# Kernel tuning notes

Measured on AMD Instinct MI355X. Metric: run time of the kernel, lower is better.

The kernel has to match this reference:

```python
import jax, jax.numpy as jnp
import numpy as np

NUM_Q = 10000
DK = 128   # dim_key (width of each memory slot and of embeddings)
DV = 64    # dim_value (number of memory slots)
B = 128
S = 200


def setup_inputs() -> dict:
    key = jax.random.key(0)
    ks = jax.random.split(key, 16)
    sc = 0.05
    return {
        "question_seq": jax.random.randint(ks[0], (B, S), 0, NUM_Q),
        "correct_seq": jax.random.randint(ks[1], (B, S), 0, 2),
        "k_emb": jax.random.normal(ks[2], (NUM_Q, DK), jnp.float32) * sc,
        "v_emb": jax.random.normal(ks[3], (2 * NUM_Q, DK), jnp.float32) * sc,
        "Mk": jax.random.normal(ks[4], (DV, DK), jnp.float32) * sc,
        "Mv0": jax.random.normal(ks[5], (DV, DK), jnp.float32) * sc,
        "fW": jax.random.normal(ks[6], (2 * DK, DK), jnp.float32) * sc,
        "fb": jnp.zeros((DK,), jnp.float32),
        "eW": jax.random.normal(ks[7], (DK, DK), jnp.float32) * sc,
        "eb": jnp.zeros((DK,), jnp.float32),
        "aW": jax.random.normal(ks[8], (DK, DK), jnp.float32) * sc,
        "ab": jnp.zeros((DK,), jnp.float32),
        "pW": jax.random.normal(ks[9], (DK, 1), jnp.float32) * sc,
        "pb": jnp.zeros((1,), jnp.float32),
    }


def reference(question_seq, correct_seq, k_emb, v_emb, Mk, Mv0, fW, fb, eW, eb, aW, ab, pW, pb):
    num_q = k_emb.shape[0]
    x = question_seq + num_q * correct_seq            # [B,S]
    k = k_emb[question_seq]                           # [B,S,DK]
    v = v_emb[x]                                      # [B,S,DK]

    w = jax.nn.softmax(jnp.einsum('bsk,vk->bsv', k, Mk), axis=-1)  # [B,S,DV]
    e = jax.nn.sigmoid(v @ eW + eb)                   # [B,S,DK]
    a = jnp.tanh(v @ aW + ab)                         # [B,S,DK]

    Mvt0 = jnp.broadcast_to(Mv0[None], (question_seq.shape[0],) + Mv0.shape)  # [B,DV,DK]

    def step(Mvt, inp):
        wt, et, at = inp                              # [B,DV],[B,DK],[B,DK]
        read = jnp.einsum('bv,bvk->bk', wt, Mvt)      # read BEFORE update (Mv[:, :-1])
        we = wt[:, :, None] * et[:, None, :]          # [B,DV,DK]
        wa = wt[:, :, None] * at[:, None, :]
        Mvt_new = Mvt * (1.0 - we) + wa
        return Mvt_new, read

    xs = (w.transpose(1, 0, 2), e.transpose(1, 0, 2), a.transpose(1, 0, 2))
    _, reads = jax.lax.scan(step, Mvt0, xs)           # reads: [S,B,DK]
    reads = reads.transpose(1, 0, 2)                  # [B,S,DK]

    f = jnp.tanh(jnp.concatenate([reads, k], axis=-1) @ fW + fb)  # [B,S,DK]
    # dropout is identity in eval mode
    predict_score = jax.nn.sigmoid(f @ pW + pb).squeeze(-1)       # [B,S]
    return predict_score
```

## Files before the change

### kernel.cpp

```cpp
#include <hip/hip_runtime.h>
#include <math.h>


typedef float f32x4 __attribute__((ext_vector_type(4)));
typedef short bf16x8 __attribute__((ext_vector_type(8)));

__device__ __forceinline__ float sigm(float x) { return 1.0f / (1.0f + __expf(-x)); }
__device__ __forceinline__ short f2bf(float x) {
    union { float f; unsigned u; } v; v.f = x;
    return (short)((v.u + 0x7FFFu + ((v.u >> 16) & 1u)) >> 16);
}

__global__ __launch_bounds__(128) void prep_kernel(
    const float* __restrict__ eW, const float* __restrict__ aW,
    const float* __restrict__ fW, const float* __restrict__ Mk,
    short* __restrict__ eWt, short* __restrict__ aWt,
    short* __restrict__ fWrt, short* __restrict__ fWkt,
    short* __restrict__ Mkb)
{
    const int t = threadIdx.x;
    if (blockIdx.x == 4) {
        for (int idx = t; idx < 1024; idx += 128) {
            const int row = idx >> 4, c8 = idx & 15;
            const float4 f0 = *(const float4*)(Mk + row * 128 + c8 * 8);
            const float4 f1 = *(const float4*)(Mk + row * 128 + c8 * 8 + 4);
            bf16x8 v;
            v[0] = f2bf(f0.x); v[1] = f2bf(f0.y); v[2] = f2bf(f0.z); v[3] = f2bf(f0.w);
            v[4] = f2bf(f1.x); v[5] = f2bf(f1.y); v[6] = f2bf(f1.z); v[7] = f2bf(f1.w);
            *(bf16x8*)(Mkb + row * 128 + c8 * 8) = v;
        }
        return;
    }
    const float* src; short* dst;
    switch (blockIdx.x) {
        case 0:  src = eW;             dst = eWt;  break;
        case 1:  src = aW;             dst = aWt;  break;
        case 2:  src = fW;             dst = fWrt; break;
        default: src = fW + 128 * 128; dst = fWkt; break;
    }
    const int n = t;
    for (int k0 = 0; k0 < 128; k0 += 8) {
        bf16x8 v;
        #pragma unroll
        for (int kk = 0; kk < 8; ++kk) v[kk] = f2bf(src[(k0 + kk) * 128 + n]);
        *(bf16x8*)(dst + n * 128 + k0) = v;
    }
}

__global__ __launch_bounds__(256) void veakf_kernel(
    const float* __restrict__ v_emb, const float* __restrict__ k_emb,
    const short* __restrict__ eWt, const short* __restrict__ aWt,
    const short* __restrict__ fWkt, const short* __restrict__ Mkb,
    const float* __restrict__ eb, const float* __restrict__ ab,
    const float* __restrict__ fb,
    int num_q, int nbe,
    float* __restrict__ e_all, float* __restrict__ a_all,
    float* __restrict__ kf_all, float* __restrict__ w_all)
{
    __shared__ __align__(16) short Ash[64 * 128];
    const int t = threadIdx.x;
    const bool ea = ((int)blockIdx.x < nbe);
    const int nrows = ea ? 2 * num_q : num_q;
    const int R0 = (ea ? blockIdx.x : blockIdx.x - nbe) * 64;
    const float* Asrc = ea ? v_emb : k_emb;

    #pragma unroll
    for (int i = 0; i < 4; ++i) {
        const int c = t + 256 * i;
        const int row = c >> 4, ch = c & 15;
        int gr = R0 + row; if (gr > nrows - 1) gr = nrows - 1;
        const float4 f0 = *(const float4*)(Asrc + (size_t)gr * 128 + ch * 8);
        const float4 f1 = *(const float4*)(Asrc + (size_t)gr * 128 + ch * 8 + 4);
        bf16x8 v;
        v[0] = f2bf(f0.x); v[1] = f2bf(f0.y); v[2] = f2bf(f0.z); v[3] = f2bf(f0.w);
        v[4] = f2bf(f1.x); v[5] = f2bf(f1.y); v[6] = f2bf(f1.z); v[7] = f2bf(f1.w);
        *(bf16x8*)&Ash[row * 128 + ((ch ^ (row & 7)) * 8)] = v;
    }
    __syncthreads();

    const int wv = t >> 6;
    const int lr = t & 15;
    const int lk = (t & 63) >> 4;
    const int arow = wv * 16 + lr;

    if (ea) {
        f32x4 acc0[8], acc1[8];
        #pragma unroll
        for (int ct = 0; ct < 8; ++ct) { acc0[ct] = (f32x4)0.f; acc1[ct] = (f32x4)0.f; }
        #pragma unroll
        for (int ks = 0; ks < 4; ++ks) {
            const int chunk = ks * 4 + lk;
            const bf16x8 af = *(const bf16x8*)&Ash[arow * 128 + ((chunk ^ (arow & 7)) * 8)];
            const int kb = ks * 32 + lk * 8;
            #pragma unroll
            for (int ct = 0; ct < 8; ++ct) {
                const int n = ct * 16 + lr;
                const bf16x8 b0 = *(const bf16x8*)(eWt + n * 128 + kb);
                const bf16x8 b1 = *(const bf16x8*)(aWt + n * 128 + kb);
                acc0[ct] = __builtin_amdgcn_mfma_f32_16x16x32_bf16(af, b0, acc0[ct], 0, 0, 0);
                acc1[ct] = __builtin_amdgcn_mfma_f32_16x16x32_bf16(af, b1, acc1[ct], 0, 0, 0);
            }
        }
        #pragma unroll
        for (int ct = 0; ct < 8; ++ct) {
            const int col = ct * 16 + lr;
            const float ebv = eb[col], abv = ab[col];
            #pragma unroll
            for (int r = 0; r < 4; ++r) {
                const int row = R0 + wv * 16 + lk * 4 + r;
                if (row < nrows) {
                    e_all[(size_t)row * 128 + col] = sigm(acc0[ct][r] + ebv);
                    a_all[(size_t)row * 128 + col] = tanhf(acc1[ct][r] + abv);
                }
            }
        }
    } else {
        f32x4 acc0[8], accw[4];
        #pragma unroll
        for (int ct = 0; ct < 8; ++ct) acc0[ct] = (f32x4)0.f;
        #pragma unroll
        for (int ct = 0; ct < 4; ++ct) accw[ct] = (f32x4)0.f;
        #pragma unroll
        for (int ks = 0; ks < 4; ++ks) {
            const int chunk = ks * 4 + lk;
            const bf16x8 af = *(const bf16x8*)&Ash[arow * 128 + ((chunk ^ (arow & 7)) * 8)];
            const int kb = ks * 32 + lk * 8;
            #pragma unroll
            for (int ct = 0; ct < 8; ++ct) {
                const int n = ct * 16 + lr;
                const bf16x8 b0 = *(const bf16x8*)(fWkt + n * 128 + kb);
                acc0[ct] = __builtin_amdgcn_mfma_f32_16x16x32_bf16(af, b0, acc0[ct], 0, 0, 0);
            }
            #pragma unroll
            for (int ct = 0; ct < 4; ++ct) {
                const int n = ct * 16 + lr;
                const bf16x8 bm = *(const bf16x8*)(Mkb + n * 128 + kb);
                accw[ct] = __builtin_amdgcn_mfma_f32_16x16x32_bf16(af, bm, accw[ct], 0, 0, 0);
            }
        }
        #pragma unroll
        for (int ct = 0; ct < 8; ++ct) {
            const int col = ct * 16 + lr;
            const float fbv = fb[col];
            #pragma unroll
            for (int r = 0; r < 4; ++r) {
                const int row = R0 + wv * 16 + lk * 4 + r;
                if (row < nrows)
                    kf_all[(size_t)row * 128 + col] = acc0[ct][r] + fbv;
            }
        }
        #pragma unroll
        for (int r = 0; r < 4; ++r) {
            const float x0 = accw[0][r], x1 = accw[1][r];
            const float x2 = accw[2][r], x3 = accw[3][r];
            float m = fmaxf(fmaxf(x0, x1), fmaxf(x2, x3));
            #pragma unroll
            for (int mk = 1; mk < 16; mk <<= 1) m = fmaxf(m, __shfl_xor(m, mk));
            const float e0 = __expf(x0 - m), e1 = __expf(x1 - m);
            const float e2 = __expf(x2 - m), e3 = __expf(x3 - m);
            float s = (e0 + e1) + (e2 + e3);
            #pragma unroll
            for (int mk = 1; mk < 16; mk <<= 1) s += __shfl_xor(s, mk);
            const float inv = 1.0f / s;
            const int row = R0 + wv * 16 + lk * 4 + r;
            if (row < nrows) {
                float* wr = w_all + (size_t)row * 64 + lr;
                wr[0]  = e0 * inv; wr[16] = e1 * inv;
                wr[32] = e2 * inv; wr[48] = e3 * inv;
            }
        }
    }
}

__global__ __launch_bounds__(256) void scan_kernel(
    const float* __restrict__ Mv0,
    const int* __restrict__ qseq, const int* __restrict__ cseq,
    const float* __restrict__ w_all, const float* __restrict__ e_all,
    const float* __restrict__ a_all, int num_q,
    unsigned short* __restrict__ reads_bf)
{
    const int t  = threadIdx.x;
    const int j  = t & 31;
    const int vg = t >> 5;
    const int cq = blockIdx.x & 3;
    const int b  = blockIdx.x >> 2;
    const int jg = cq * 32 + j;

    float Mv[8];
    #pragma unroll
    for (int i = 0; i < 8; ++i) Mv[i] = Mv0[(vg * 8 + i) * 128 + jg];

    __shared__ float wb[2][8][64];
    __shared__ float ebuf[2][8][32];
    __shared__ float abuf[2][8][32];
    __shared__ float part[2][8][8][32];
    __shared__ int sq[200], sx[200];

    if (t < 200) {
        const int q = qseq[b * 200 + t];
        const int c = cseq[b * 200 + t];
        sq[t] = q * 16;
        sx[t] = (q + num_q * c) * 32 + cq * 8;
    }
    __syncthreads();

    const float4* w4 = (const float4*)w_all;
    const float4* e4 = (const float4*)e_all;
    const float4* a4 = (const float4*)a_all;
    unsigned short* rp = reads_bf + (size_t)b * 200 * 128 + jg;

    float4 rg;
    if (t < 128)      { rg = w4[sq[t >> 4] + (t & 15)];               ((float4*)wb[0])[t] = rg; }
    else if (t < 192) { const int u = t - 128; rg = e4[sx[u >> 3] + (u & 7)]; ((float4*)ebuf[0])[u] = rg; }
    else              { const int u = t - 192; rg = a4[sx[u >> 3] + (u & 7)]; ((float4*)abuf[0])[u] = rg; }
    __syncthreads();

    int cb = 0, pbuf = 0;
    for (int c = 0; c < 25; ++c) {
        if (c < 24) {
            const int s0 = (c + 1) * 8;
            if (t < 128)      rg = w4[sq[s0 + (t >> 4)] + (t & 15)];
            else if (t < 192) { const int u = t - 128; rg = e4[sx[s0 + (u >> 3)] + (u & 7)]; }
            else              { const int u = t - 192; rg = a4[sx[s0 + (u >> 3)] + (u & 7)]; }
        }
        #pragma unroll
        for (int st = 0; st < 8; ++st) {
            const float e_j = ebuf[cb][st][j];
            const float a_j = abuf[cb][st][j];
            const float* wrow = &wb[cb][st][vg * 8];
            float r0 = 0.f, r1 = 0.f, r2 = 0.f, r3 = 0.f;
            #pragma unroll
            for (int v4i = 0; v4i < 2; ++v4i) {
                const float4 w4v = *(const float4*)&wrow[v4i * 4];
                const int v = v4i * 4;
                r0 = fmaf(w4v.x, Mv[v + 0], r0);
                Mv[v + 0] = fmaf(w4v.x, fmaf(-Mv[v + 0], e_j, a_j), Mv[v + 0]);
                r1 = fmaf(w4v.y, Mv[v + 1], r1);
                Mv[v + 1] = fmaf(w4v.y, fmaf(-Mv[v + 1], e_j, a_j), Mv[v + 1]);
                r2 = fmaf(w4v.z, Mv[v + 2], r2);
                Mv[v + 2] = fmaf(w4v.z, fmaf(-Mv[v + 2], e_j, a_j), Mv[v + 2]);
                r3 = fmaf(w4v.w, Mv[v + 3], r3);
                Mv[v + 3] = fmaf(w4v.w, fmaf(-Mv[v + 3], e_j, a_j), Mv[v + 3]);
            }
            part[pbuf][st][vg][j] = (r0 + r1) + (r2 + r3);
        }
        if (c < 24) {
            if (t < 128)      ((float4*)wb[cb ^ 1])[t] = rg;
            else if (t < 192) ((float4*)ebuf[cb ^ 1])[t - 128] = rg;
            else              ((float4*)abuf[cb ^ 1])[t - 192] = rg;
        }
        __syncthreads();
        {
            const int st = t >> 5, jr = t & 31;
            const float* pp = &part[pbuf][st][0][jr];
            float r = 0.f;
            #pragma unroll
            for (int g = 0; g < 8; ++g) r += pp[g * 32];
            reads_bf[(size_t)b * 200 * 128 + (size_t)(c * 8 + st) * 128 + cq * 32 + jr]
                = (unsigned short)f2bf(r);
        }
        cb ^= 1; pbuf ^= 1;
    }
    (void)rp;
}

__global__ __launch_bounds__(256) void out_kernel(
    const int* __restrict__ qseq,
    const unsigned short* __restrict__ reads_bf,
    const short* __restrict__ fWrt, const float* __restrict__ kf_all,
    const float* __restrict__ pW, const float* __restrict__ pb,
    int ntok, float* __restrict__ out)
{
    __shared__ __align__(16) short Ash[64 * 128];
    __shared__ int qi[64];
    const int t = threadIdx.x;
    const int R0 = blockIdx.x * 64;
    if (t < 64) { int r = R0 + t; qi[t] = qseq[r < ntok ? r : ntok - 1]; }
    #pragma unroll
    for (int i = 0; i < 4; ++i) {
        const int c = t + 256 * i;
        const int row = c >> 4, ch = c & 15;
        int gr = R0 + row; if (gr > ntok - 1) gr = ntok - 1;
        const bf16x8 v = *(const bf16x8*)(reads_bf + (size_t)gr * 128 + ch * 8);
        *(bf16x8*)&Ash[row * 128 + ((ch ^ (row & 7)) * 8)] = v;
    }
    __syncthreads();

    const int wv = t >> 6;
    const int lr = t & 15;
    const int lk = (t & 63) >> 4;
    const int arow = wv * 16 + lr;

    f32x4 acc[8];
    #pragma unroll
    for (int ct = 0; ct < 8; ++ct) {
        const int col = ct * 16 + lr;
        #pragma unroll
        for (int r = 0; r < 4; ++r) {
            const int q = qi[wv * 16 + lk * 4 + r];
            acc[ct][r] = kf_all[(size_t)q * 128 + col];
        }
    }
    #pragma unroll
    for (int ks = 0; ks < 4; ++ks) {
        const int chunk = ks * 4 + lk;
        const bf16x8 af = *(const bf16x8*)&Ash[arow * 128 + ((chunk ^ (arow & 7)) * 8)];
        const int kb = ks * 32 + lk * 8;
        #pragma unroll
        for (int ct = 0; ct < 8; ++ct) {
            const int n = ct * 16 + lr;
            const bf16x8 bfr = *(const bf16x8*)(fWrt + n * 128 + kb);
            acc[ct] = __builtin_amdgcn_mfma_f32_16x16x32_bf16(af, bfr, acc[ct], 0, 0, 0);
        }
    }
    const float pb0 = pb[0];
    float s0 = 0.f, s1 = 0.f, s2 = 0.f, s3 = 0.f;
    #pragma unroll
    for (int ct = 0; ct < 8; ++ct) {
        const float pw = pW[ct * 16 + lr];
        s0 = fmaf(tanhf(acc[ct][0]), pw, s0);
        s1 = fmaf(tanhf(acc[ct][1]), pw, s1);
        s2 = fmaf(tanhf(acc[ct][2]), pw, s2);
        s3 = fmaf(tanhf(acc[ct][3]), pw, s3);
    }
    #pragma unroll
    for (int off = 1; off < 16; off <<= 1) {
        s0 += __shfl_xor(s0, off);
        s1 += __shfl_xor(s1, off);
        s2 += __shfl_xor(s2, off);
        s3 += __shfl_xor(s3, off);
    }
    if (lr == 0) {
        const int row = R0 + wv * 16 + lk * 4;
        if (row + 0 < ntok) out[row + 0] = sigm(s0 + pb0);
        if (row + 1 < ntok) out[row + 1] = sigm(s1 + pb0);
        if (row + 2 < ntok) out[row + 2] = sigm(s2 + pb0);
        if (row + 3 < ntok) out[row + 3] = sigm(s3 + pb0);
    }
}

extern "C" void kernel_launch(void* const* d_in, const int* in_sizes, int n_in,
                              void* d_out, int out_size, void* d_ws, size_t ws_size,
                              hipStream_t stream)
{
    const int*   qseq  = (const int*)d_in[0];
    const int*   cseq  = (const int*)d_in[1];
    const float* k_emb = (const float*)d_in[2];
    const float* v_emb = (const float*)d_in[3];
    const float* Mk    = (const float*)d_in[4];
    const float* Mv0   = (const float*)d_in[5];
    const float* fW    = (const float*)d_in[6];
    const float* fb    = (const float*)d_in[7];
    const float* eW    = (const float*)d_in[8];
    const float* eb    = (const float*)d_in[9];
    const float* aW    = (const float*)d_in[10];
    const float* ab    = (const float*)d_in[11];
    const float* pW    = (const float*)d_in[12];
    const float* pb    = (const float*)d_in[13];

    const int num_q = in_sizes[2] / 128;
    const int ntok  = in_sizes[0];
    const int Bb    = ntok / 200;
    const int NV    = 2 * num_q;

    float* ws = (float*)d_ws;
    float* w_all  = ws;
    float* e_all  = w_all  + (size_t)num_q * 64;
    float* a_all  = e_all  + (size_t)NV * 128;
    float* kf_all = a_all  + (size_t)NV * 128;
    short* eWt    = (short*)(kf_all + (size_t)num_q * 128);
    short* aWt    = eWt  + 128 * 128;
    short* fWrt   = aWt  + 128 * 128;
    short* fWkt   = fWrt + 128 * 128;
    short* Mkb    = fWkt + 128 * 128;
    unsigned short* reads_bf = (unsigned short*)(Mkb + 64 * 128);

    prep_kernel<<<5, 128, 0, stream>>>(eW, aW, fW, Mk, eWt, aWt, fWrt, fWkt, Mkb);
    const int nbe = (NV + 63) / 64, nbk = (num_q + 63) / 64;
    veakf_kernel<<<nbe + nbk, 256, 0, stream>>>(v_emb, k_emb, eWt, aWt, fWkt, Mkb,
                                                eb, ab, fb, num_q, nbe,
                                                e_all, a_all, kf_all, w_all);
    scan_kernel<<<Bb * 4, 256, 0, stream>>>(Mv0, qseq, cseq, w_all, e_all, a_all,
                                            num_q, reads_bf);
    out_kernel<<<(ntok + 63) / 64, 256, 0, stream>>>(qseq, reads_bf, fWrt, kf_all,
                                                     pW, pb, ntok, (float*)d_out);
}
```

Baseline: 77.56 us.

## Stage weight matrices in LDS and load activation fragments directly to registers

```diff
diff --git a/kernel.cpp b/kernel.cpp
--- a/kernel.cpp
+++ b/kernel.cpp
@@ -11,7 +11,7 @@
     return (short)((v.u + 0x7FFFu + ((v.u >> 16) & 1u)) >> 16);
 }
 
-__global__ __launch_bounds__(128) void prep_kernel(
+__global__ __launch_bounds__(256) void prep_kernel(
     const float* __restrict__ eW, const float* __restrict__ aW,
     const float* __restrict__ fW, const float* __restrict__ Mk,
     short* __restrict__ eWt, short* __restrict__ aWt,
@@ -20,7 +20,7 @@
 {
     const int t = threadIdx.x;
     if (blockIdx.x == 4) {
-        for (int idx = t; idx < 1024; idx += 128) {
+        for (int idx = t; idx < 1024; idx += 256) {
             const int row = idx >> 4, c8 = idx & 15;
             const float4 f0 = *(const float4*)(Mk + row * 128 + c8 * 8);
             const float4 f1 = *(const float4*)(Mk + row * 128 + c8 * 8 + 4);
@@ -38,8 +38,9 @@
         case 2:  src = fW;             dst = fWrt; break;
         default: src = fW + 128 * 128; dst = fWkt; break;
     }
-    const int n = t;
-    for (int k0 = 0; k0 < 128; k0 += 8) {
+    const int n  = t & 127;
+    const int kh = (t >> 7) * 64;
+    for (int k0 = kh; k0 < kh + 64; k0 += 8) {
         bf16x8 v;
         #pragma unroll
         for (int kk = 0; kk < 8; ++kk) v[kk] = f2bf(src[(k0 + kk) * 128 + n]);
@@ -57,87 +58,74 @@
     float* __restrict__ e_all, float* __restrict__ a_all,
     float* __restrict__ kf_all, float* __restrict__ w_all)
 {
-    __shared__ __align__(16) short Ash[64 * 128];
+    __shared__ __align__(16) short Bsh[128 * 128];
     const int t = threadIdx.x;
     const bool ea = ((int)blockIdx.x < nbe);
     const int nrows = ea ? 2 * num_q : num_q;
-    const int R0 = (ea ? blockIdx.x : blockIdx.x - nbe) * 64;
+    const int R0 = (ea ? (int)blockIdx.x : (int)blockIdx.x - nbe) * 64;
     const float* Asrc = ea ? v_emb : k_emb;
-
-    #pragma unroll
-    for (int i = 0; i < 4; ++i) {
-        const int c = t + 256 * i;
-        const int row = c >> 4, ch = c & 15;
-        int gr = R0 + row; if (gr > nrows - 1) gr = nrows - 1;
-        const float4 f0 = *(const float4*)(Asrc + (size_t)gr * 128 + ch * 8);
-        const float4 f1 = *(const float4*)(Asrc + (size_t)gr * 128 + ch * 8 + 4);
-        bf16x8 v;
-        v[0] = f2bf(f0.x); v[1] = f2bf(f0.y); v[2] = f2bf(f0.z); v[3] = f2bf(f0.w);
-        v[4] = f2bf(f1.x); v[5] = f2bf(f1.y); v[6] = f2bf(f1.z); v[7] = f2bf(f1.w);
-        *(bf16x8*)&Ash[row * 128 + ((ch ^ (row & 7)) * 8)] = v;
-    }
-    __syncthreads();
 
     const int wv = t >> 6;
     const int lr = t & 15;
     const int lk = (t & 63) >> 4;
     const int arow = wv * 16 + lr;
-
+    int gr = R0 + arow; if (gr > nrows - 1) gr = nrows - 1;
+
+    float4 a0[4], a1[4];
+    #pragma unroll
+    for (int ks = 0; ks < 4; ++ks) {
+        const int off = (ks * 4 + lk) * 8;
+        a0[ks] = *(const float4*)(Asrc + (size_t)gr * 128 + off);
+        a1[ks] = *(const float4*)(Asrc + (size_t)gr * 128 + off + 4);
+    }
+    {
+        const short* B1 = ea ? eWt : fWkt;
+        #pragma unroll
+        for (int i = 0; i < 8; ++i) {
+            const int c = t + 256 * i;
+            const int row = c >> 4, ch = c & 15;
+            *(bf16x8*)&Bsh[row * 128 + ((ch ^ (row & 7)) * 8)] =
+                *(const bf16x8*)(B1 + row * 128 + ch * 8);
+        }
+    }
+    bf16x8 af[4];
+    #pragma unroll
+    for (int ks = 0; ks < 4; ++ks) {
+        bf16x8 v;
+        v[0] = f2bf(a0[ks].x); v[1] = f2bf(a0[ks].y);
+        v[2] = f2bf(a0[ks].z); v[3] = f2bf(a0[ks].w);
+        v[4] = f2bf(a1[ks].x); v[5] = f2bf(a1[ks].y);
+        v[6] = f2bf(a1[ks].z); v[7] = f2bf(a1[ks].w);
+        af[ks] = v;
+    }
+    __syncthreads();
+
+    f32x4 acc[8];
+    #pragma unroll
+    for (int ct = 0; ct < 8; ++ct) acc[ct] = (f32x4)0.f;
+    #pragma unroll
+    for (int ks = 0; ks < 4; ++ks) {
+        const int chunk = ks * 4 + lk;
+        #pragma unroll
+        for (int ct = 0; ct < 8; ++ct) {
+            const int n = ct * 16 + lr;
+            const bf16x8 b = *(const bf16x8*)&Bsh[n * 128 + ((chunk ^ (n & 7)) * 8)];
+            acc[ct] = __builtin_amdgcn_mfma_f32_16x16x32_bf16(af[ks], b, acc[ct], 0, 0, 0);
+        }
+    }
     if (ea) {
-        f32x4 acc0[8], acc1[8];
-        #pragma unroll
-        for (int ct = 0; ct < 8; ++ct) { acc0[ct] = (f32x4)0.f; acc1[ct] = (f32x4)0.f; }
-        #pragma unroll
-        for (int ks = 0; ks < 4; ++ks) {
-            const int chunk = ks * 4 + lk;
-            const bf16x8 af = *(const bf16x8*)&Ash[arow * 128 + ((chunk ^ (arow & 7)) * 8)];
-            const int kb = ks * 32 + lk * 8;
-            #pragma unroll
-            for (int ct = 0; ct < 8; ++ct) {
-                const int n = ct * 16 + lr;
-                const bf16x8 b0 = *(const bf16x8*)(eWt + n * 128 + kb);
-                const bf16x8 b1 = *(const bf16x8*)(aWt + n * 128 + kb);
-                acc0[ct] = __builtin_amdgcn_mfma_f32_16x16x32_bf16(af, b0, acc0[ct], 0, 0, 0);
-                acc1[ct] = __builtin_amdgcn_mfma_f32_16x16x32_bf16(af, b1, acc1[ct], 0, 0, 0);
-            }
-        }
         #pragma unroll
         for (int ct = 0; ct < 8; ++ct) {
             const int col = ct * 16 + lr;
-            const float ebv = eb[col], abv = ab[col];
+            const float ebv = eb[col];
             #pragma unroll
             for (int r = 0; r < 4; ++r) {
                 const int row = R0 + wv * 16 + lk * 4 + r;
-                if (row < nrows) {
-                    e_all[(size_t)row * 128 + col] = sigm(acc0[ct][r] + ebv);
-                    a_all[(size_t)row * 128 + col] = tanhf(acc1[ct][r] + abv);
-                }
+                if (row < nrows)
+                    e_all[(size_t)row * 128 + col] = sigm(acc[ct][r] + ebv);
             }
         }
     } else {
-        f32x4 acc0[8], accw[4];
-        #pragma unroll
-        for (int ct = 0; ct < 8; ++ct) acc0[ct] = (f32x4)0.f;
-        #pragma unroll
-        for (int ct = 0; ct < 4; ++ct) accw[ct] = (f32x4)0.f;
-        #pragma unroll
-        for (int ks = 0; ks < 4; ++ks) {
-            const int chunk = ks * 4 + lk;
-            const bf16x8 af = *(const bf16x8*)&Ash[arow * 128 + ((chunk ^ (arow & 7)) * 8)];
-            const int kb = ks * 32 + lk * 8;
-            #pragma unroll
-            for (int ct = 0; ct < 8; ++ct) {
-                const int n = ct * 16 + lr;
-                const bf16x8 b0 = *(const bf16x8*)(fWkt + n * 128 + kb);
-                acc0[ct] = __builtin_amdgcn_mfma_f32_16x16x32_bf16(af, b0, acc0[ct], 0, 0, 0);
-            }
-            #pragma unroll
-            for (int ct = 0; ct < 4; ++ct) {
-                const int n = ct * 16 + lr;
-                const bf16x8 bm = *(const bf16x8*)(Mkb + n * 128 + kb);
-                accw[ct] = __builtin_amdgcn_mfma_f32_16x16x32_bf16(af, bm, accw[ct], 0, 0, 0);
-            }
-        }
         #pragma unroll
         for (int ct = 0; ct < 8; ++ct) {
             const int col = ct * 16 + lr;
@@ -146,7 +134,67 @@
             for (int r = 0; r < 4; ++r) {
                 const int row = R0 + wv * 16 + lk * 4 + r;
                 if (row < nrows)
-                    kf_all[(size_t)row * 128 + col] = acc0[ct][r] + fbv;
+                    kf_all[(size_t)row * 128 + col] = acc[ct][r] + fbv;
+            }
+        }
+    }
+    __syncthreads();
+
+    if (ea) {
+        #pragma unroll
+        for (int i = 0; i < 8; ++i) {
+            const int c = t + 256 * i;
+            const int row = c >> 4, ch = c & 15;
+            *(bf16x8*)&Bsh[row * 128 + ((ch ^ (row & 7)) * 8)] =
+                *(const bf16x8*)(aWt + row * 128 + ch * 8);
+        }
+    } else {
+        #pragma unroll
+        for (int i = 0; i < 4; ++i) {
+            const int c = t + 256 * i;
+            const int row = c >> 4, ch = c & 15;
+            *(bf16x8*)&Bsh[row * 128 + ((ch ^ (row & 7)) * 8)] =
+                *(const bf16x8*)(Mkb + row * 128 + ch * 8);
+        }
+    }
+    __syncthreads();
+
+    if (ea) {
+        #pragma unroll
+        for (int ct = 0; ct < 8; ++ct) acc[ct] = (f32x4)0.f;
+        #pragma unroll
+        for (int ks = 0; ks < 4; ++ks) {
+            const int chunk = ks * 4 + lk;
+            #pragma unroll
+            for (int ct = 0; ct < 8; ++ct) {
+                const int n = ct * 16 + lr;
+                const bf16x8 b = *(const bf16x8*)&Bsh[n * 128 + ((chunk ^ (n & 7)) * 8)];
+                acc[ct] = __builtin_amdgcn_mfma_f32_16x16x32_bf16(af[ks], b, acc[ct], 0, 0, 0);
+            }
+        }
+        #pragma unroll
+        for (int ct = 0; ct < 8; ++ct) {
+            const int col = ct * 16 + lr;
+            const float abv = ab[col];
+            #pragma unroll
+            for (int r = 0; r < 4; ++r) {
+                const int row = R0 + wv * 16 + lk * 4 + r;
+                if (row < nrows)
+                    a_all[(size_t)row * 128 + col] = tanhf(acc[ct][r] + abv);
+            }
+        }
+    } else {
+        f32x4 accw[4];
+        #pragma unroll
+        for (int ct = 0; ct < 4; ++ct) accw[ct] = (f32x4)0.f;
+        #pragma unroll
+        for (int ks = 0; ks < 4; ++ks) {
+            const int chunk = ks * 4 + lk;
+            #pragma unroll
+            for (int ct = 0; ct < 4; ++ct) {
+                const int n = ct * 16 + lr;
+                const bf16x8 b = *(const bf16x8*)&Bsh[n * 128 + ((chunk ^ (n & 7)) * 8)];
+                accw[ct] = __builtin_amdgcn_mfma_f32_16x16x32_bf16(af[ks], b, accw[ct], 0, 0, 0);
             }
         }
         #pragma unroll
@@ -207,10 +255,9 @@
     const float4* w4 = (const float4*)w_all;
     const float4* e4 = (const float4*)e_all;
     const float4* a4 = (const float4*)a_all;
-    unsigned short* rp = reads_bf + (size_t)b * 200 * 128 + jg;
 
     float4 rg;
-    if (t < 128)      { rg = w4[sq[t >> 4] + (t & 15)];               ((float4*)wb[0])[t] = rg; }
+    if (t < 128)      { rg = w4[sq[t >> 4] + (t & 15)];                       ((float4*)wb[0])[t] = rg; }
     else if (t < 192) { const int u = t - 128; rg = e4[sx[u >> 3] + (u & 7)]; ((float4*)ebuf[0])[u] = rg; }
     else              { const int u = t - 192; rg = a4[sx[u >> 3] + (u & 7)]; ((float4*)abuf[0])[u] = rg; }
     __syncthreads();
@@ -261,7 +308,6 @@
         }
         cb ^= 1; pbuf ^= 1;
     }
-    (void)rp;
 }
 
 __global__ __launch_bounds__(256) void out_kernel(
@@ -375,7 +421,7 @@
     short* Mkb    = fWkt + 128 * 128;
     unsigned short* reads_bf = (unsigned short*)(Mkb + 64 * 128);
 
-    prep_kernel<<<5, 128, 0, stream>>>(eW, aW, fW, Mk, eWt, aWt, fWrt, fWkt, Mkb);
+    prep_kernel<<<5, 256, 0, stream>>>(eW, aW, fW, Mk, eWt, aWt, fWrt, fWkt, Mkb);
     const int nbe = (NV + 63) / 64, nbk = (num_q + 63) / 64;
     veakf_kernel<<<nbe + nbk, 256, 0, stream>>>(v_emb, k_emb, eWt, aWt, fWkt, Mkb,
                                                 eb, ab, fb, num_q, nbe,
```

After: 69.46 us. 1.12x faster.
